# Kernel tuning notes

Hardware: AMD Instinct MI355X
Metric: run time of the kernel (lower is better)

Reference implementation:

```python
import jax, jax.numpy as jnp
import numpy as np

LA, LB, D = 4096, 4096, 1024

def setup_inputs() -> dict:
    key = jax.random.key(0)
    ka, kb = jax.random.split(key)
    a_hat = jax.random.normal(ka, (LA, D), dtype=jnp.float32)
    b_hat = jax.random.normal(kb, (LB, D), dtype=jnp.float32)
    return {"a_hat": a_hat, "b_hat": b_hat}

def _m_vector(v_hat, v_wave):
    # concat along dim 0, matching torch.concat(..., dim=0)
    return jnp.concatenate((v_hat, v_wave, v_hat - v_wave, v_hat * v_wave), axis=0)

def reference(a_hat, b_hat):
    # energy: [La, Lb]
    energy = jnp.matmul(a_hat, b_hat.T)
    # softmax over columns (dim 1) -> attend over b rows
    wave_a = jnp.matmul(jax.nn.softmax(energy, axis=1), b_hat)      # [La, D]
    # softmax over rows (dim 0), transposed -> attend over a rows
    wave_b = jnp.matmul(jax.nn.softmax(energy, axis=0).T, a_hat)    # [Lb, D]
    m_a = _m_vector(a_hat, wave_a)   # [4*La, D]
    m_b = _m_vector(b_hat, wave_b)   # [4*Lb, D]
    return (m_a, m_b)
```

## Files before the change

kernel.cpp:

```cpp
#include <hip/hip_runtime.h>
#include <cstdint>
#include <cstddef>

#define LA 4096
#define LB 4096
#define DD 1024

typedef unsigned short u16;
typedef short bf16x8 __attribute__((ext_vector_type(8)));
typedef float f32x4 __attribute__((ext_vector_type(4)));

__device__ __forceinline__ u16 f2bf(float f) {
  unsigned u = __builtin_bit_cast(unsigned, f);
  u += 0x7fffu + ((u >> 16) & 1u);
  return (u16)(u >> 16);
}
__device__ __forceinline__ float bf2f(u16 h) {
  return __builtin_bit_cast(float, (unsigned)h << 16);
}
__device__ __forceinline__ bf16x8 pack8(float4 a, float4 b) {
  bf16x8 r;
  r[0] = (short)f2bf(a.x); r[1] = (short)f2bf(a.y);
  r[2] = (short)f2bf(a.z); r[3] = (short)f2bf(a.w);
  r[4] = (short)f2bf(b.x); r[5] = (short)f2bf(b.y);
  r[6] = (short)f2bf(b.z); r[7] = (short)f2bf(b.w);
  return r;
}
__device__ __forceinline__ void async16(const void* g, void* l) {
  __builtin_amdgcn_global_load_lds(
      (const __attribute__((address_space(1))) unsigned int*)g,
      (__attribute__((address_space(3))) unsigned int*)l, 16, 0, 0);
}

__global__ __launch_bounds__(256) void split_ab(const float* __restrict__ A,
                                                const float* __restrict__ B,
                                                u16* __restrict__ Ahi, u16* __restrict__ Alo,
                                                u16* __restrict__ Bhi, u16* __restrict__ Blo) {
  const int side = blockIdx.x >> 11;
  const size_t idx = ((size_t)(blockIdx.x & 2047) * 256 + threadIdx.x) * 8;
  const float* src = side ? B : A;
  u16* dh = side ? Bhi : Ahi;
  u16* dl = side ? Blo : Alo;
  const float4 a = *(const float4*)&src[idx];
  const float4 b = *(const float4*)&src[idx + 4];
  float v[8] = {a.x, a.y, a.z, a.w, b.x, b.y, b.z, b.w};
  bf16x8 hi, lo;
#pragma unroll
  for (int i = 0; i < 8; ++i) {
    const u16 h = f2bf(v[i]);
    hi[i] = (short)h;
    lo[i] = (short)f2bf(v[i] - bf2f(h));
  }
  *(bf16x8*)&dh[idx] = hi;
  *(bf16x8*)&dl[idx] = lo;
}

__global__ __launch_bounds__(256) void tr_f32(const float* __restrict__ in,
                                              u16* __restrict__ out,
                                              int R, int C) {
  __shared__ u16 t[32][33];
  const int c0 = blockIdx.x * 32, r0 = blockIdx.y * 32;
  const int tid = threadIdx.x;
  const int lr = tid >> 3, lc = (tid & 7) * 4;
  const float4 v = *(const float4*)&in[(size_t)(r0 + lr) * C + c0 + lc];
  t[lr][lc + 0] = f2bf(v.x); t[lr][lc + 1] = f2bf(v.y);
  t[lr][lc + 2] = f2bf(v.z); t[lr][lc + 3] = f2bf(v.w);
  __syncthreads();
  ushort4 w;
  w.x = t[lc + 0][lr]; w.y = t[lc + 1][lr]; w.z = t[lc + 2][lr]; w.w = t[lc + 3][lr];
  *(ushort4*)&out[(size_t)(c0 + lr) * R + r0 + lc] = w;
}

__global__ __launch_bounds__(256) void gemm_energy(const u16* __restrict__ Ahi,
                                                   const u16* __restrict__ Alo,
                                                   const u16* __restrict__ Bhi,
                                                   const u16* __restrict__ Blo,
                                                   float* __restrict__ E) {
  __shared__ u16 lah[128 * 32], lal[128 * 32], lbh[128 * 32], lbl[128 * 32];
  const int j0 = blockIdx.x * 128;
  const int i0 = blockIdx.y * 128;
  const int tid = threadIdx.x;
  const int lane = tid & 63, quad = lane >> 4, lq = lane & 15;
  const int wave = tid >> 6;
  const int wm = (wave & 1) * 64, wn = (wave >> 1) * 64;
  f32x4 acc[4][4] = {};
  for (int kt = 0; kt < DD; kt += 32) {
    if (kt) __syncthreads();
#pragma unroll
    for (int r = 0; r < 2; ++r) {
      const int chunk = wave * 128 + r * 64 + lane;
      const int row = chunk >> 2;
      const int kc = (chunk & 3) * 8;
      const int lofs = (wave * 128 + r * 64) * 16;
      const size_t ga = (size_t)(i0 + row) * DD + kt + kc;
      const size_t gb = (size_t)(j0 + row) * DD + kt + kc;
      async16(Ahi + ga, (char*)lah + lofs);
      async16(Alo + ga, (char*)lal + lofs);
      async16(Bhi + gb, (char*)lbh + lofs);
      async16(Blo + gb, (char*)lbl + lofs);
    }
    __syncthreads();
    bf16x8 fah[4], fal[4], fbh[4], fbl[4];
#pragma unroll
    for (int f = 0; f < 4; ++f) {
      fah[f] = *(const bf16x8*)&lah[(wm + f * 16 + lq) * 32 + quad * 8];
      fal[f] = *(const bf16x8*)&lal[(wm + f * 16 + lq) * 32 + quad * 8];
      fbh[f] = *(const bf16x8*)&lbh[(wn + f * 16 + lq) * 32 + quad * 8];
      fbl[f] = *(const bf16x8*)&lbl[(wn + f * 16 + lq) * 32 + quad * 8];
    }
#pragma unroll
    for (int fm = 0; fm < 4; ++fm)
#pragma unroll
      for (int fn = 0; fn < 4; ++fn) {
        acc[fm][fn] = __builtin_amdgcn_mfma_f32_16x16x32_bf16(fal[fm], fbh[fn], acc[fm][fn], 0, 0, 0);
        acc[fm][fn] = __builtin_amdgcn_mfma_f32_16x16x32_bf16(fah[fm], fbl[fn], acc[fm][fn], 0, 0, 0);
        acc[fm][fn] = __builtin_amdgcn_mfma_f32_16x16x32_bf16(fah[fm], fbh[fn], acc[fm][fn], 0, 0, 0);
      }
  }
#pragma unroll
  for (int fm = 0; fm < 4; ++fm)
#pragma unroll
    for (int fn = 0; fn < 4; ++fn)
#pragma unroll
      for (int r = 0; r < 4; ++r) {
        const int gi = i0 + wm + fm * 16 + quad * 4 + r;
        const int gj = j0 + wn + fn * 16 + lq;
        E[(size_t)gi * LB + gj] = acc[fm][fn][r];
      }
}

__global__ __launch_bounds__(256) void row_softmax_pa(const float* __restrict__ E,
                                                      float* __restrict__ rinv,
                                                      u16* __restrict__ P,
                                                      float* __restrict__ wa) {
  __shared__ float red[8];
  const int row = blockIdx.x, tid = threadIdx.x;
  const float* e = E + (size_t)row * LB;
  float4 v[4];
#pragma unroll
  for (int c = 0; c < 4; ++c) v[c] = *(const float4*)&e[(c * 256 + tid) * 4];
  float m = -__builtin_inff();
#pragma unroll
  for (int c = 0; c < 4; ++c)
    m = fmaxf(m, fmaxf(fmaxf(v[c].x, v[c].y), fmaxf(v[c].z, v[c].w)));
#pragma unroll
  for (int o = 32; o > 0; o >>= 1) m = fmaxf(m, __shfl_down(m, o));
  if ((tid & 63) == 0) red[tid >> 6] = m;
  __syncthreads();
  m = fmaxf(fmaxf(red[0], red[1]), fmaxf(red[2], red[3]));
  float s = 0.f;
#pragma unroll
  for (int c = 0; c < 4; ++c)
    s += __expf(v[c].x - m) + __expf(v[c].y - m) + __expf(v[c].z - m) + __expf(v[c].w - m);
#pragma unroll
  for (int o = 32; o > 0; o >>= 1) s += __shfl_down(s, o);
  if ((tid & 63) == 0) red[4 + (tid >> 6)] = s;
  __syncthreads();
  if (tid == 0) rinv[row] = 1.f / (red[4] + red[5] + red[6] + red[7]);
#pragma unroll
  for (int c = 0; c < 4; ++c) {
    ushort4 w;
    w.x = f2bf(__expf(v[c].x - m));
    w.y = f2bf(__expf(v[c].y - m));
    w.z = f2bf(__expf(v[c].z - m));
    w.w = f2bf(__expf(v[c].w - m));
    *(ushort4*)&P[(size_t)row * LB + (c * 256 + tid) * 4] = w;
  }
  float4 z = {0.f, 0.f, 0.f, 0.f};
  *(float4*)&wa[(size_t)row * DD + tid * 4] = z;
}

__global__ __launch_bounds__(256) void col_partial(const float* __restrict__ E,
                                                   float* __restrict__ pmax,
                                                   float* __restrict__ psum) {
  const int c = blockIdx.x * 256 + threadIdx.x;
  const int rg = blockIdx.y;
  const float* e = E + (size_t)rg * 128 * LB + c;
  float m = -__builtin_inff(), s = 0.f;
#pragma unroll 4
  for (int r = 0; r < 128; ++r) {
    const float x = e[(size_t)r * LB];
    const float nm = fmaxf(m, x);
    s = s * __expf(m - nm) + __expf(x - nm);
    m = nm;
  }
  pmax[rg * LB + c] = m;
  psum[rg * LB + c] = s;
}

__global__ __launch_bounds__(256) void col_combine(const float* __restrict__ pmax,
                                                   const float* __restrict__ psum,
                                                   float* __restrict__ cmax,
                                                   float* __restrict__ cinv) {
  const int c = blockIdx.x * 256 + threadIdx.x;
  float m = -__builtin_inff(), s = 0.f;
#pragma unroll 4
  for (int g = 0; g < 32; ++g) {
    const float pm = pmax[g * LB + c], ps = psum[g * LB + c];
    const float nm = fmaxf(m, pm);
    s = s * __expf(m - nm) + ps * __expf(pm - nm);
    m = nm;
  }
  cmax[c] = m;
  cinv[c] = 1.f / s;
}

__global__ __launch_bounds__(256) void make_pb(const float* __restrict__ E,
                                               const float* __restrict__ cmax,
                                               u16* __restrict__ P) {
  __shared__ u16 t[32][33];
  const int j0 = blockIdx.x * 32;
  const int i0 = blockIdx.y * 32;
  const int tid = threadIdx.x;
  const int lr = tid >> 3, lc = (tid & 7) * 4;
  const float4 v = *(const float4*)&E[(size_t)(i0 + lr) * LB + j0 + lc];
  const float4 cm = *(const float4*)&cmax[j0 + lc];
  t[lr][lc + 0] = f2bf(__expf(v.x - cm.x));
  t[lr][lc + 1] = f2bf(__expf(v.y - cm.y));
  t[lr][lc + 2] = f2bf(__expf(v.z - cm.z));
  t[lr][lc + 3] = f2bf(__expf(v.w - cm.w));
  __syncthreads();
  ushort4 w;
  w.x = t[lc + 0][lr]; w.y = t[lc + 1][lr]; w.z = t[lc + 2][lr]; w.w = t[lc + 3][lr];
  *(ushort4*)&P[(size_t)(j0 + lr) * LA + i0 + lc] = w;
}

template <int ATOMIC>
__global__ __launch_bounds__(256) void gemm_pv(const u16* __restrict__ P,
                                               const u16* __restrict__ Vt,
                                               const float* __restrict__ inv,
                                               float* __restrict__ W0,
                                               float* __restrict__ W1) {
  __shared__ u16 lds_a[128 * 32];
  __shared__ u16 lds_b[128 * 32];
  const int n0 = blockIdx.x * 128;
  const int i0 = blockIdx.y * 128;
  const int kz = blockIdx.z;
  const int tid = threadIdx.x;
  const int lane = tid & 63, quad = lane >> 4, lq = lane & 15;
  const int wave = tid >> 6;
  const int wm = (wave & 1) * 64, wn = (wave >> 1) * 64;
  f32x4 acc[4][4] = {};
  for (int t = 0; t < 64; ++t) {
    const int kt = kz * 2048 + t * 32;
    if (t) __syncthreads();
#pragma unroll
    for (int r = 0; r < 2; ++r) {
      const int chunk = wave * 128 + r * 64 + lane;
      const int row = chunk >> 2;
      const int kc = (chunk & 3) * 8;
      const int lofs = (wave * 128 + r * 64) * 16;
      async16(P + (size_t)(i0 + row) * 4096 + kt + kc, (char*)lds_a + lofs);
      async16(Vt + (size_t)(n0 + row) * 4096 + kt + kc, (char*)lds_b + lofs);
    }
    __syncthreads();
    bf16x8 af[4], bfr[4];
#pragma unroll
    for (int f = 0; f < 4; ++f) {
      af[f]  = *(const bf16x8*)&lds_a[(wm + f * 16 + lq) * 32 + quad * 8];
      bfr[f] = *(const bf16x8*)&lds_b[(wn + f * 16 + lq) * 32 + quad * 8];
    }
#pragma unroll
    for (int fm = 0; fm < 4; ++fm)
#pragma unroll
      for (int fn = 0; fn < 4; ++fn)
        acc[fm][fn] = __builtin_amdgcn_mfma_f32_16x16x32_bf16(af[fm], bfr[fn], acc[fm][fn], 0, 0, 0);
  }
  float* W = ATOMIC ? W0 : (kz ? W1 : W0);
#pragma unroll
  for (int fm = 0; fm < 4; ++fm)
#pragma unroll
    for (int r = 0; r < 4; ++r) {
      const int gm = i0 + wm + fm * 16 + quad * 4 + r;
      const float sc = inv[gm];
#pragma unroll
      for (int fn = 0; fn < 4; ++fn) {
        const int gn = n0 + wn + fn * 16 + lq;
        if (ATOMIC)
          unsafeAtomicAdd(&W[(size_t)gm * DD + gn], acc[fm][fn][r] * sc);
        else
          W[(size_t)gm * DD + gn] = acc[fm][fn][r] * sc;
      }
    }
}

__global__ __launch_bounds__(256) void finish(const float* __restrict__ Ain,
                                              const float* __restrict__ Bin,
                                              const float* __restrict__ p1,
                                              float* __restrict__ out) {
  const int side = blockIdx.x >> 11;
  const int blk = blockIdx.x & 2047;
  const size_t idx = ((size_t)blk * 256 + threadIdx.x) * 8;
  const size_t S = (size_t)LA * DD;
  const float* src = side ? Bin : Ain;
  float* ob = out + (size_t)side * 4 * S;
  const float4 a0 = *(const float4*)&src[idx];
  const float4 a1 = *(const float4*)&src[idx + 4];
  float4 w0 = *(const float4*)&ob[S + idx];
  float4 w1 = *(const float4*)&ob[S + idx + 4];
  if (side) {
    const float4 q0 = *(const float4*)&p1[idx];
    const float4 q1 = *(const float4*)&p1[idx + 4];
    w0.x += q0.x; w0.y += q0.y; w0.z += q0.z; w0.w += q0.w;
    w1.x += q1.x; w1.y += q1.y; w1.z += q1.z; w1.w += q1.w;
    *(float4*)&ob[S + idx] = w0;
    *(float4*)&ob[S + idx + 4] = w1;
  }
  float4 s0, s1, m0, m1;
  s0.x = a0.x - w0.x; s0.y = a0.y - w0.y; s0.z = a0.z - w0.z; s0.w = a0.w - w0.w;
  s1.x = a1.x - w1.x; s1.y = a1.y - w1.y; s1.z = a1.z - w1.z; s1.w = a1.w - w1.w;
  m0.x = a0.x * w0.x; m0.y = a0.y * w0.y; m0.z = a0.z * w0.z; m0.w = a0.w * w0.w;
  m1.x = a1.x * w1.x; m1.y = a1.y * w1.y; m1.z = a1.z * w1.z; m1.w = a1.w * w1.w;
  *(float4*)&ob[idx] = a0;            *(float4*)&ob[idx + 4] = a1;
  *(float4*)&ob[2 * S + idx] = s0;    *(float4*)&ob[2 * S + idx + 4] = s1;
  *(float4*)&ob[3 * S + idx] = m0;    *(float4*)&ob[3 * S + idx + 4] = m1;
}

extern "C" void kernel_launch(void* const* d_in, const int* in_sizes, int n_in,
                              void* d_out, int out_size, void* d_ws, size_t ws_size,
                              hipStream_t stream) {
  const float* A = (const float*)d_in[0];
  const float* B = (const float*)d_in[1];
  float* out = (float*)d_out;
  const size_t S = (size_t)LA * DD;

  float* pmax = out;
  float* psum = pmax + 131072;
  float* rmax = psum + 131072;
  float* rinv = rmax + 4096;
  float* cmax = rinv + 4096;
  float* cinv = cmax + 4096;
  u16*   Bt   = (u16*)(out + 1048576);
  u16*   Ahi  = (u16*)(out + 2 * S);
  u16*   Alo  = Ahi + S;
  u16*   Bhi  = Alo + S;
  u16*   Blo  = Bhi + S;
  u16*   P    = (u16*)(out + 2 * S);
  float* E    = out + 4 * S;
  u16*   At   = (u16*)(out + 4 * S);
  float* wave_a = out + S;
  float* wave_b = out + 5 * S;
  float* pB1    = out + 6 * S;

  split_ab<<<dim3(4096), 256, 0, stream>>>(A, B, Ahi, Alo, Bhi, Blo);
  gemm_energy<<<dim3(LB / 128, LA / 128), 256, 0, stream>>>(Ahi, Alo, Bhi, Blo, E);

  row_softmax_pa<<<dim3(LA), 256, 0, stream>>>(E, rinv, P, wave_a);
  col_partial<<<dim3(LB / 256, 32), 256, 0, stream>>>(E, pmax, psum);
  col_combine<<<dim3(LB / 256), 256, 0, stream>>>(pmax, psum, cmax, cinv);

  tr_f32<<<dim3(DD / 32, LB / 32), 256, 0, stream>>>(B, Bt, LB, DD);
  gemm_pv<1><<<dim3(DD / 128, LA / 128, 2), 256, 0, stream>>>(P, Bt, rinv, wave_a, nullptr);

  make_pb<<<dim3(LB / 32, LA / 32), 256, 0, stream>>>(E, cmax, P);
  tr_f32<<<dim3(DD / 32, LA / 32), 256, 0, stream>>>(A, At, LA, DD);
  gemm_pv<0><<<dim3(DD / 128, LB / 128, 2), 256, 0, stream>>>(P, At, cinv, wave_b, pB1);

  finish<<<dim3(4096), 256, 0, stream>>>(A, B, pB1, out);
}
```

Measured before the change: 466.4 us.

## Unify GEMMs into a 256x256 double-buffered swizzled MFMA kernel with K-concatenated split-bf16

Replaces the energy GEMM and both PV GEMMs with one templated 256x256-tile, 512-thread kernel. It uses double-buffered async global-to-LDS loads, XOR-swizzled LDS layout, block index remapping and setprio around the MFMAs. The hi/lo split for the energy GEMM is folded into the K dimension: A is stored as [hi,hi,lo] and B as [hi,lo,hi], so a single K=3072 GEMM computes all three cross products. The PV GEMMs switch to 4-way split-K with atomic accumulation, which needs a zeroing pass for wave_b and adds atomic traffic and LDS/register pressure.

```diff
diff --git a/kernel.cpp b/kernel.cpp
--- a/kernel.cpp
+++ b/kernel.cpp
@@ -18,14 +18,6 @@
 __device__ __forceinline__ float bf2f(u16 h) {
   return __builtin_bit_cast(float, (unsigned)h << 16);
 }
-__device__ __forceinline__ bf16x8 pack8(float4 a, float4 b) {
-  bf16x8 r;
-  r[0] = (short)f2bf(a.x); r[1] = (short)f2bf(a.y);
-  r[2] = (short)f2bf(a.z); r[3] = (short)f2bf(a.w);
-  r[4] = (short)f2bf(b.x); r[5] = (short)f2bf(b.y);
-  r[6] = (short)f2bf(b.z); r[7] = (short)f2bf(b.w);
-  return r;
-}
 __device__ __forceinline__ void async16(const void* g, void* l) {
   __builtin_amdgcn_global_load_lds(
       (const __attribute__((address_space(1))) unsigned int*)g,
@@ -34,13 +26,12 @@
 
 __global__ __launch_bounds__(256) void split_ab(const float* __restrict__ A,
                                                 const float* __restrict__ B,
-                                                u16* __restrict__ Ahi, u16* __restrict__ Alo,
-                                                u16* __restrict__ Bhi, u16* __restrict__ Blo) {
+                                                u16* __restrict__ Ap,
+                                                u16* __restrict__ Bp) {
   const int side = blockIdx.x >> 11;
   const size_t idx = ((size_t)(blockIdx.x & 2047) * 256 + threadIdx.x) * 8;
   const float* src = side ? B : A;
-  u16* dh = side ? Bhi : Ahi;
-  u16* dl = side ? Blo : Alo;
+  u16* dst = side ? Bp : Ap;
   const float4 a = *(const float4*)&src[idx];
   const float4 b = *(const float4*)&src[idx + 4];
   float v[8] = {a.x, a.y, a.z, a.w, b.x, b.y, b.z, b.w};
@@ -51,8 +42,12 @@
     hi[i] = (short)h;
     lo[i] = (short)f2bf(v[i] - bf2f(h));
   }
-  *(bf16x8*)&dh[idx] = hi;
-  *(bf16x8*)&dl[idx] = lo;
+  const size_t row = idx >> 10;
+  const size_t k = idx & 1023;
+  u16* base = dst + row * 3072 + k;
+  *(bf16x8*)&base[0] = hi;
+  *(bf16x8*)&base[side ? 2048 : 1024] = hi;
+  *(bf16x8*)&base[side ? 1024 : 2048] = lo;
 }
 
 __global__ __launch_bounds__(256) void tr_f32(const float* __restrict__ in,
@@ -71,62 +66,111 @@
   *(ushort4*)&out[(size_t)(c0 + lr) * R + r0 + lc] = w;
 }
 
-__global__ __launch_bounds__(256) void gemm_energy(const u16* __restrict__ Ahi,
-                                                   const u16* __restrict__ Alo,
-                                                   const u16* __restrict__ Bhi,
-                                                   const u16* __restrict__ Blo,
-                                                   float* __restrict__ E) {
-  __shared__ u16 lah[128 * 32], lal[128 * 32], lbh[128 * 32], lbl[128 * 32];
-  const int j0 = blockIdx.x * 128;
-  const int i0 = blockIdx.y * 128;
+#define STAGE8(buf, ktile)                                                   \
+  do {                                                                       \
+    const size_t kb = (size_t)(ktile) * 128;                                 \
+    _Pragma("unroll") for (int l = 0; l < 4; ++l)                            \
+        async16(Ag8 + aoff[l] + kb, &lA[buf][ldst[l]]);                      \
+    _Pragma("unroll") for (int l = 0; l < 4; ++l)                            \
+        async16(Bg8 + boff[l] + kb, &lB[buf][ldst[l]]);                      \
+  } while (0)
+
+template <int ATOMIC>
+__global__ __launch_bounds__(512, 2) void gemm8(const u16* __restrict__ Ag,
+                                                const u16* __restrict__ Bg,
+                                                const float* __restrict__ inv,
+                                                float* __restrict__ C,
+                                                const int K, const int ldc,
+                                                const int Ksub) {
+  __shared__ u16 lA[2][256 * 64];
+  __shared__ u16 lB[2][256 * 64];
+  const int gx = gridDim.x;
+  const int nxy = gx * gridDim.y;
+  int lin = blockIdx.y * gx + blockIdx.x;
+  lin = (lin & 7) * (nxy >> 3) + (lin >> 3);
+  const int j0 = (lin % gx) * 256;
+  const int i0 = (lin / gx) * 256;
   const int tid = threadIdx.x;
   const int lane = tid & 63, quad = lane >> 4, lq = lane & 15;
   const int wave = tid >> 6;
-  const int wm = (wave & 1) * 64, wn = (wave >> 1) * 64;
-  f32x4 acc[4][4] = {};
-  for (int kt = 0; kt < DD; kt += 32) {
-    if (kt) __syncthreads();
-#pragma unroll
-    for (int r = 0; r < 2; ++r) {
-      const int chunk = wave * 128 + r * 64 + lane;
-      const int row = chunk >> 2;
-      const int kc = (chunk & 3) * 8;
-      const int lofs = (wave * 128 + r * 64) * 16;
-      const size_t ga = (size_t)(i0 + row) * DD + kt + kc;
-      const size_t gb = (size_t)(j0 + row) * DD + kt + kc;
-      async16(Ahi + ga, (char*)lah + lofs);
-      async16(Alo + ga, (char*)lal + lofs);
-      async16(Bhi + gb, (char*)lbh + lofs);
-      async16(Blo + gb, (char*)lbl + lofs);
+  const int wr = wave >> 2, wc = wave & 3;
+  const char* Ag8 = (const char*)Ag;
+  const char* Bg8 = (const char*)Bg;
+
+  size_t aoff[4], boff[4];
+  int ldst[4];
+#pragma unroll
+  for (int l = 0; l < 4; ++l) {
+    const int d = l * 8192 + tid * 16;
+    const int row = d >> 7;
+    const int cb = (d & 127) ^ ((row & 7) << 4);
+    aoff[l] = ((size_t)(i0 + row) * K + (size_t)blockIdx.z * Ksub) * 2 + cb;
+    boff[l] = ((size_t)(j0 + row) * K + (size_t)blockIdx.z * Ksub) * 2 + cb;
+    ldst[l] = (l * 8192 + wave * 1024) >> 1;
+  }
+
+  f32x4 acc[8][4] = {};
+  const int NT = Ksub >> 6;
+  STAGE8(0, 0);
+  STAGE8(1, 1);
+
+  for (int t = 0; t < NT; ++t) {
+    const int cur = t & 1;
+    if (t < NT - 1)
+      asm volatile("s_waitcnt vmcnt(8)" ::: "memory");
+    else
+      asm volatile("s_waitcnt vmcnt(0)" ::: "memory");
+    __builtin_amdgcn_s_barrier();
+    const char* bA = (const char*)&lA[cur][0];
+    const char* bB = (const char*)&lB[cur][0];
+#pragma unroll
+    for (int ks = 0; ks < 2; ++ks) {
+      bf16x8 bfrag[4];
+#pragma unroll
+      for (int f = 0; f < 4; ++f) {
+        const int row = wc * 64 + f * 16 + lq;
+        bfrag[f] = *(const bf16x8*)(bB + row * 128 +
+                                    ((ks * 64 + quad * 16) ^ ((lq & 7) << 4)));
+      }
+#pragma unroll
+      for (int mh = 0; mh < 2; ++mh) {
+        bf16x8 afrag[4];
+#pragma unroll
+        for (int f = 0; f < 4; ++f) {
+          const int row = wr * 128 + (mh * 4 + f) * 16 + lq;
+          afrag[f] = *(const bf16x8*)(bA + row * 128 +
+                                      ((ks * 64 + quad * 16) ^ ((lq & 7) << 4)));
+        }
+        __builtin_amdgcn_s_setprio(1);
+#pragma unroll
+        for (int fm = 0; fm < 4; ++fm)
+#pragma unroll
+          for (int fn = 0; fn < 4; ++fn)
+            acc[mh * 4 + fm][fn] = __builtin_amdgcn_mfma_f32_16x16x32_bf16(
+                afrag[fm], bfrag[fn], acc[mh * 4 + fm][fn], 0, 0, 0);
+        __builtin_amdgcn_s_setprio(0);
+      }
     }
-    __syncthreads();
-    bf16x8 fah[4], fal[4], fbh[4], fbl[4];
-#pragma unroll
-    for (int f = 0; f < 4; ++f) {
-      fah[f] = *(const bf16x8*)&lah[(wm + f * 16 + lq) * 32 + quad * 8];
-      fal[f] = *(const bf16x8*)&lal[(wm + f * 16 + lq) * 32 + quad * 8];
-      fbh[f] = *(const bf16x8*)&lbh[(wn + f * 16 + lq) * 32 + quad * 8];
-      fbl[f] = *(const bf16x8*)&lbl[(wn + f * 16 + lq) * 32 + quad * 8];
+    __builtin_amdgcn_s_barrier();
+    if (t + 2 < NT) STAGE8(cur, t + 2);
+  }
+
+#pragma unroll
+  for (int fm = 0; fm < 8; ++fm) {
+    const int gi = i0 + wr * 128 + fm * 16 + quad * 4;
+#pragma unroll
+    for (int r = 0; r < 4; ++r) {
+#pragma unroll
+      for (int fn = 0; fn < 4; ++fn) {
+        const int gj = j0 + wc * 64 + fn * 16 + lq;
+        float* p = &C[(size_t)(gi + r) * ldc + gj];
+        if (ATOMIC)
+          unsafeAtomicAdd(p, acc[fm][fn][r] * inv[gi + r]);
+        else
+          *p = acc[fm][fn][r];
+      }
     }
-#pragma unroll
-    for (int fm = 0; fm < 4; ++fm)
-#pragma unroll
-      for (int fn = 0; fn < 4; ++fn) {
-        acc[fm][fn] = __builtin_amdgcn_mfma_f32_16x16x32_bf16(fal[fm], fbh[fn], acc[fm][fn], 0, 0, 0);
-        acc[fm][fn] = __builtin_amdgcn_mfma_f32_16x16x32_bf16(fah[fm], fbl[fn], acc[fm][fn], 0, 0, 0);
-        acc[fm][fn] = __builtin_amdgcn_mfma_f32_16x16x32_bf16(fah[fm], fbh[fn], acc[fm][fn], 0, 0, 0);
-      }
-  }
-#pragma unroll
-  for (int fm = 0; fm < 4; ++fm)
-#pragma unroll
-    for (int fn = 0; fn < 4; ++fn)
-#pragma unroll
-      for (int r = 0; r < 4; ++r) {
-        const int gi = i0 + wm + fm * 16 + quad * 4 + r;
-        const int gj = j0 + wn + fn * 16 + lq;
-        E[(size_t)gi * LB + gj] = acc[fm][fn][r];
-      }
+  }
 }
 
 __global__ __launch_bounds__(256) void row_softmax_pa(const float* __restrict__ E,
@@ -225,68 +269,15 @@
   *(ushort4*)&P[(size_t)(j0 + lr) * LA + i0 + lc] = w;
 }
 
-template <int ATOMIC>
-__global__ __launch_bounds__(256) void gemm_pv(const u16* __restrict__ P,
-                                               const u16* __restrict__ Vt,
-                                               const float* __restrict__ inv,
-                                               float* __restrict__ W0,
-                                               float* __restrict__ W1) {
-  __shared__ u16 lds_a[128 * 32];
-  __shared__ u16 lds_b[128 * 32];
-  const int n0 = blockIdx.x * 128;
-  const int i0 = blockIdx.y * 128;
-  const int kz = blockIdx.z;
-  const int tid = threadIdx.x;
-  const int lane = tid & 63, quad = lane >> 4, lq = lane & 15;
-  const int wave = tid >> 6;
-  const int wm = (wave & 1) * 64, wn = (wave >> 1) * 64;
-  f32x4 acc[4][4] = {};
-  for (int t = 0; t < 64; ++t) {
-    const int kt = kz * 2048 + t * 32;
-    if (t) __syncthreads();
-#pragma unroll
-    for (int r = 0; r < 2; ++r) {
-      const int chunk = wave * 128 + r * 64 + lane;
-      const int row = chunk >> 2;
-      const int kc = (chunk & 3) * 8;
-      const int lofs = (wave * 128 + r * 64) * 16;
-      async16(P + (size_t)(i0 + row) * 4096 + kt + kc, (char*)lds_a + lofs);
-      async16(Vt + (size_t)(n0 + row) * 4096 + kt + kc, (char*)lds_b + lofs);
-    }
-    __syncthreads();
-    bf16x8 af[4], bfr[4];
-#pragma unroll
-    for (int f = 0; f < 4; ++f) {
-      af[f]  = *(const bf16x8*)&lds_a[(wm + f * 16 + lq) * 32 + quad * 8];
-      bfr[f] = *(const bf16x8*)&lds_b[(wn + f * 16 + lq) * 32 + quad * 8];
-    }
-#pragma unroll
-    for (int fm = 0; fm < 4; ++fm)
-#pragma unroll
-      for (int fn = 0; fn < 4; ++fn)
-        acc[fm][fn] = __builtin_amdgcn_mfma_f32_16x16x32_bf16(af[fm], bfr[fn], acc[fm][fn], 0, 0, 0);
-  }
-  float* W = ATOMIC ? W0 : (kz ? W1 : W0);
-#pragma unroll
-  for (int fm = 0; fm < 4; ++fm)
-#pragma unroll
-    for (int r = 0; r < 4; ++r) {
-      const int gm = i0 + wm + fm * 16 + quad * 4 + r;
-      const float sc = inv[gm];
-#pragma unroll
-      for (int fn = 0; fn < 4; ++fn) {
-        const int gn = n0 + wn + fn * 16 + lq;
-        if (ATOMIC)
-          unsafeAtomicAdd(&W[(size_t)gm * DD + gn], acc[fm][fn][r] * sc);
-        else
-          W[(size_t)gm * DD + gn] = acc[fm][fn][r] * sc;
-      }
-    }
+__global__ __launch_bounds__(256) void wb_zero(float* __restrict__ w) {
+  const size_t idx = ((size_t)blockIdx.x * 256 + threadIdx.x) * 8;
+  const float4 z = {0.f, 0.f, 0.f, 0.f};
+  *(float4*)&w[idx] = z;
+  *(float4*)&w[idx + 4] = z;
 }
 
 __global__ __launch_bounds__(256) void finish(const float* __restrict__ Ain,
                                               const float* __restrict__ Bin,
-                                              const float* __restrict__ p1,
                                               float* __restrict__ out) {
   const int side = blockIdx.x >> 11;
   const int blk = blockIdx.x & 2047;
@@ -296,16 +287,8 @@
   float* ob = out + (size_t)side * 4 * S;
   const float4 a0 = *(const float4*)&src[idx];
   const float4 a1 = *(const float4*)&src[idx + 4];
-  float4 w0 = *(const float4*)&ob[S + idx];
-  float4 w1 = *(const float4*)&ob[S + idx + 4];
-  if (side) {
-    const float4 q0 = *(const float4*)&p1[idx];
-    const float4 q1 = *(const float4*)&p1[idx + 4];
-    w0.x += q0.x; w0.y += q0.y; w0.z += q0.z; w0.w += q0.w;
-    w1.x += q1.x; w1.y += q1.y; w1.z += q1.z; w1.w += q1.w;
-    *(float4*)&ob[S + idx] = w0;
-    *(float4*)&ob[S + idx + 4] = w1;
-  }
+  const float4 w0 = *(const float4*)&ob[S + idx];
+  const float4 w1 = *(const float4*)&ob[S + idx + 4];
   float4 s0, s1, m0, m1;
   s0.x = a0.x - w0.x; s0.y = a0.y - w0.y; s0.z = a0.z - w0.z; s0.w = a0.w - w0.w;
   s1.x = a1.x - w1.x; s1.y = a1.y - w1.y; s1.z = a1.z - w1.z; s1.w = a1.w - w1.w;
@@ -331,30 +314,28 @@
   float* cmax = rinv + 4096;
   float* cinv = cmax + 4096;
   u16*   Bt   = (u16*)(out + 1048576);
-  u16*   Ahi  = (u16*)(out + 2 * S);
-  u16*   Alo  = Ahi + S;
-  u16*   Bhi  = Alo + S;
-  u16*   Blo  = Bhi + S;
+  u16*   Ap   = (u16*)(out + S);
+  u16*   Bp   = Ap + (size_t)LA * 3072;
   u16*   P    = (u16*)(out + 2 * S);
   float* E    = out + 4 * S;
   u16*   At   = (u16*)(out + 4 * S);
   float* wave_a = out + S;
   float* wave_b = out + 5 * S;
-  float* pB1    = out + 6 * S;
-
-  split_ab<<<dim3(4096), 256, 0, stream>>>(A, B, Ahi, Alo, Bhi, Blo);
-  gemm_energy<<<dim3(LB / 128, LA / 128), 256, 0, stream>>>(Ahi, Alo, Bhi, Blo, E);
+
+  split_ab<<<dim3(4096), 256, 0, stream>>>(A, B, Ap, Bp);
+  gemm8<0><<<dim3(LB / 256, LA / 256), 512, 0, stream>>>(Ap, Bp, nullptr, E, 3072, LB, 3072);
 
   row_softmax_pa<<<dim3(LA), 256, 0, stream>>>(E, rinv, P, wave_a);
   col_partial<<<dim3(LB / 256, 32), 256, 0, stream>>>(E, pmax, psum);
   col_combine<<<dim3(LB / 256), 256, 0, stream>>>(pmax, psum, cmax, cinv);
 
   tr_f32<<<dim3(DD / 32, LB / 32), 256, 0, stream>>>(B, Bt, LB, DD);
-  gemm_pv<1><<<dim3(DD / 128, LA / 128, 2), 256, 0, stream>>>(P, Bt, rinv, wave_a, nullptr);
+  gemm8<1><<<dim3(DD / 256, LA / 256, 4), 512, 0, stream>>>(P, Bt, rinv, wave_a, 4096, DD, 1024);
 
   make_pb<<<dim3(LB / 32, LA / 32), 256, 0, stream>>>(E, cmax, P);
   tr_f32<<<dim3(DD / 32, LA / 32), 256, 0, stream>>>(A, At, LA, DD);
-  gemm_pv<0><<<dim3(DD / 128, LB / 128, 2), 256, 0, stream>>>(P, At, cinv, wave_b, pB1);
-
-  finish<<<dim3(4096), 256, 0, stream>>>(A, B, pB1, out);
-}
+  wb_zero<<<dim3(2048), 256, 0, stream>>>(wave_b);
+  gemm8<1><<<dim3(DD / 256, LB / 256, 4), 512, 0, stream>>>(P, At, cinv, wave_b, 4096, DD, 1024);
+
+  finish<<<dim3(4096), 256, 0, stream>>>(A, B, out);
+}
```

After: 506.0 us. 1.09x slower.

## Fuse column softmax partials into energy GEMM epilogue and merge prep kernels

Applied to the files above, without the earlier changes.

The energy GEMM epilogue now computes per-column max and sum-of-exp partials for each 128-row tile straight from the accumulators, using shuffles and a small shared reduction, so the separate col_partial pass that re-read the full energy matrix is removed. The split into hi/lo bf16 and the B transpose are merged into one prep launch. This saves a 64MB read of E and two launches. In exchange the GEMM epilogue gains extra exp work, a barrier and some shared memory, which may lower occupancy.

```diff
diff --git a/kernel.cpp b/kernel.cpp
--- a/kernel.cpp
+++ b/kernel.cpp
@@ -18,41 +18,51 @@
 __device__ __forceinline__ float bf2f(u16 h) {
   return __builtin_bit_cast(float, (unsigned)h << 16);
 }
-__device__ __forceinline__ bf16x8 pack8(float4 a, float4 b) {
-  bf16x8 r;
-  r[0] = (short)f2bf(a.x); r[1] = (short)f2bf(a.y);
-  r[2] = (short)f2bf(a.z); r[3] = (short)f2bf(a.w);
-  r[4] = (short)f2bf(b.x); r[5] = (short)f2bf(b.y);
-  r[6] = (short)f2bf(b.z); r[7] = (short)f2bf(b.w);
-  return r;
-}
 __device__ __forceinline__ void async16(const void* g, void* l) {
   __builtin_amdgcn_global_load_lds(
       (const __attribute__((address_space(1))) unsigned int*)g,
       (__attribute__((address_space(3))) unsigned int*)l, 16, 0, 0);
 }
 
-__global__ __launch_bounds__(256) void split_ab(const float* __restrict__ A,
-                                                const float* __restrict__ B,
-                                                u16* __restrict__ Ahi, u16* __restrict__ Alo,
-                                                u16* __restrict__ Bhi, u16* __restrict__ Blo) {
-  const int side = blockIdx.x >> 11;
-  const size_t idx = ((size_t)(blockIdx.x & 2047) * 256 + threadIdx.x) * 8;
-  const float* src = side ? B : A;
-  u16* dh = side ? Bhi : Ahi;
-  u16* dl = side ? Blo : Alo;
-  const float4 a = *(const float4*)&src[idx];
-  const float4 b = *(const float4*)&src[idx + 4];
-  float v[8] = {a.x, a.y, a.z, a.w, b.x, b.y, b.z, b.w};
-  bf16x8 hi, lo;
-#pragma unroll
-  for (int i = 0; i < 8; ++i) {
-    const u16 h = f2bf(v[i]);
-    hi[i] = (short)h;
-    lo[i] = (short)f2bf(v[i] - bf2f(h));
-  }
-  *(bf16x8*)&dh[idx] = hi;
-  *(bf16x8*)&dl[idx] = lo;
+__global__ __launch_bounds__(256) void prep(const float* __restrict__ A,
+                                            const float* __restrict__ B,
+                                            u16* __restrict__ Ahi, u16* __restrict__ Alo,
+                                            u16* __restrict__ Bhi, u16* __restrict__ Blo,
+                                            u16* __restrict__ Bt) {
+  __shared__ u16 t[32][33];
+  const int bx = blockIdx.x;
+  const int tid = threadIdx.x;
+  if (bx < 4096) {
+    const int side = bx >> 11;
+    const size_t idx = ((size_t)(bx & 2047) * 256 + tid) * 8;
+    const float* src = side ? B : A;
+    u16* dh = side ? Bhi : Ahi;
+    u16* dl = side ? Blo : Alo;
+    const float4 a = *(const float4*)&src[idx];
+    const float4 b = *(const float4*)&src[idx + 4];
+    float v[8] = {a.x, a.y, a.z, a.w, b.x, b.y, b.z, b.w};
+    bf16x8 hi, lo;
+#pragma unroll
+    for (int i = 0; i < 8; ++i) {
+      const u16 h = f2bf(v[i]);
+      hi[i] = (short)h;
+      lo[i] = (short)f2bf(v[i] - bf2f(h));
+    }
+    *(bf16x8*)&dh[idx] = hi;
+    *(bf16x8*)&dl[idx] = lo;
+  } else {
+    const int blk = bx - 4096;
+    const int c0 = (blk & 31) * 32;
+    const int r0 = (blk >> 5) * 32;
+    const int lr = tid >> 3, lc = (tid & 7) * 4;
+    const float4 v = *(const float4*)&B[(size_t)(r0 + lr) * DD + c0 + lc];
+    t[lr][lc + 0] = f2bf(v.x); t[lr][lc + 1] = f2bf(v.y);
+    t[lr][lc + 2] = f2bf(v.z); t[lr][lc + 3] = f2bf(v.w);
+    __syncthreads();
+    ushort4 w;
+    w.x = t[lc + 0][lr]; w.y = t[lc + 1][lr]; w.z = t[lc + 2][lr]; w.w = t[lc + 3][lr];
+    *(ushort4*)&Bt[(size_t)(c0 + lr) * LB + r0 + lc] = w;
+  }
 }
 
 __global__ __launch_bounds__(256) void tr_f32(const float* __restrict__ in,
@@ -75,8 +85,11 @@
                                                    const u16* __restrict__ Alo,
                                                    const u16* __restrict__ Bhi,
                                                    const u16* __restrict__ Blo,
-                                                   float* __restrict__ E) {
+                                                   float* __restrict__ E,
+                                                   float* __restrict__ pmax,
+                                                   float* __restrict__ psum) {
   __shared__ u16 lah[128 * 32], lal[128 * 32], lbh[128 * 32], lbl[128 * 32];
+  __shared__ float cred[4][4][16][2];
   const int j0 = blockIdx.x * 128;
   const int i0 = blockIdx.y * 128;
   const int tid = threadIdx.x;
@@ -127,6 +140,42 @@
         const int gj = j0 + wn + fn * 16 + lq;
         E[(size_t)gi * LB + gj] = acc[fm][fn][r];
       }
+  const int rg = i0 >> 7;
+#pragma unroll
+  for (int fn = 0; fn < 4; ++fn) {
+    float m = acc[0][fn][0];
+#pragma unroll
+    for (int fm = 0; fm < 4; ++fm)
+#pragma unroll
+      for (int r = 0; r < 4; ++r) m = fmaxf(m, acc[fm][fn][r]);
+    float s = 0.f;
+#pragma unroll
+    for (int fm = 0; fm < 4; ++fm)
+#pragma unroll
+      for (int r = 0; r < 4; ++r) s += __expf(acc[fm][fn][r] - m);
+#pragma unroll
+    for (int mask = 16; mask <= 32; mask <<= 1) {
+      const float om = __shfl_xor(m, mask);
+      const float os = __shfl_xor(s, mask);
+      const float nm = fmaxf(m, om);
+      s = s * __expf(m - nm) + os * __expf(om - nm);
+      m = nm;
+    }
+    if (quad == 0) { cred[wave][fn][lq][0] = m; cred[wave][fn][lq][1] = s; }
+  }
+  __syncthreads();
+  if ((wave & 1) == 0 && quad == 0) {
+#pragma unroll
+    for (int fn = 0; fn < 4; ++fn) {
+      const float m1 = cred[wave][fn][lq][0], s1 = cred[wave][fn][lq][1];
+      const float m2 = cred[wave + 1][fn][lq][0], s2 = cred[wave + 1][fn][lq][1];
+      const float nm = fmaxf(m1, m2);
+      const float s = s1 * __expf(m1 - nm) + s2 * __expf(m2 - nm);
+      const int c = j0 + wn + fn * 16 + lq;
+      pmax[rg * LB + c] = nm;
+      psum[rg * LB + c] = s;
+    }
+  }
 }
 
 __global__ __launch_bounds__(256) void row_softmax_pa(const float* __restrict__ E,
@@ -168,24 +217,6 @@
   }
   float4 z = {0.f, 0.f, 0.f, 0.f};
   *(float4*)&wa[(size_t)row * DD + tid * 4] = z;
-}
-
-__global__ __launch_bounds__(256) void col_partial(const float* __restrict__ E,
-                                                   float* __restrict__ pmax,
-                                                   float* __restrict__ psum) {
-  const int c = blockIdx.x * 256 + threadIdx.x;
-  const int rg = blockIdx.y;
-  const float* e = E + (size_t)rg * 128 * LB + c;
-  float m = -__builtin_inff(), s = 0.f;
-#pragma unroll 4
-  for (int r = 0; r < 128; ++r) {
-    const float x = e[(size_t)r * LB];
-    const float nm = fmaxf(m, x);
-    s = s * __expf(m - nm) + __expf(x - nm);
-    m = nm;
-  }
-  pmax[rg * LB + c] = m;
-  psum[rg * LB + c] = s;
 }
 
 __global__ __launch_bounds__(256) void col_combine(const float* __restrict__ pmax,
@@ -342,14 +373,13 @@
   float* wave_b = out + 5 * S;
   float* pB1    = out + 6 * S;
 
-  split_ab<<<dim3(4096), 256, 0, stream>>>(A, B, Ahi, Alo, Bhi, Blo);
-  gemm_energy<<<dim3(LB / 128, LA / 128), 256, 0, stream>>>(Ahi, Alo, Bhi, Blo, E);
+  prep<<<dim3(8192), 256, 0, stream>>>(A, B, Ahi, Alo, Bhi, Blo, Bt);
+
+  gemm_energy<<<dim3(LB / 128, LA / 128), 256, 0, stream>>>(Ahi, Alo, Bhi, Blo, E, pmax, psum);
 
   row_softmax_pa<<<dim3(LA), 256, 0, stream>>>(E, rinv, P, wave_a);
-  col_partial<<<dim3(LB / 256, 32), 256, 0, stream>>>(E, pmax, psum);
   col_combine<<<dim3(LB / 256), 256, 0, stream>>>(pmax, psum, cmax, cinv);
 
-  tr_f32<<<dim3(DD / 32, LB / 32), 256, 0, stream>>>(B, Bt, LB, DD);
   gemm_pv<1><<<dim3(DD / 128, LA / 128, 2), 256, 0, stream>>>(P, Bt, rinv, wave_a, nullptr);
 
   make_pb<<<dim3(LB / 32, LA / 32), 256, 0, stream>>>(E, cmax, P);
```

New measurement: 442.2 us. 1.05x faster.
